# Optimization experiments

Hardware: AMD Instinct MI355X
Metric: run time of the kernel (lower is better)

The kernel has to match this reference:

```python
import math
import jax, jax.numpy as jnp
import numpy as np

N_HEAD = 8


def setup_inputs() -> dict:
    key = jax.random.key(0)
    ks = jax.random.split(key, 9)
    B, S, D = 4, 2048, 512
    s = 1.0 / math.sqrt(D)
    return {
        "x": jax.random.normal(ks[0], (B, S, D), jnp.float32),
        "Wq": jax.random.normal(ks[1], (D, D), jnp.float32) * s,
        "bq": jax.random.normal(ks[2], (D,), jnp.float32) * s,
        "Wk": jax.random.normal(ks[3], (D, D), jnp.float32) * s,
        "bk": jax.random.normal(ks[4], (D,), jnp.float32) * s,
        "Wv": jax.random.normal(ks[5], (D, D), jnp.float32) * s,
        "bv": jax.random.normal(ks[6], (D,), jnp.float32) * s,
        "Wo": jax.random.normal(ks[7], (D, D), jnp.float32) * s,
        "bo": jax.random.normal(ks[8], (D,), jnp.float32) * s,
    }


def reference(x, Wq, bq, Wk, bk, Wv, bv, Wo, bo):
    B, S, D = x.shape
    H = N_HEAD
    hd = D // H
    # projections -> [B, H, S, hd]
    def split_heads(y):
        return y.reshape(B, S, H, hd).transpose(0, 2, 1, 3)
    q = split_heads(x @ Wq + bq)
    k = split_heads(x @ Wk + bk)
    v = split_heads(x @ Wv + bv)
    scale = 1.0 / math.sqrt(hd)
    scores = jnp.einsum("bhqd,bhkd->bhqk", q, k) * scale  # [B,H,S,S]
    attn = jax.nn.softmax(scores, axis=-1)
    ctx = jnp.einsum("bhqk,bhkd->bhqd", attn, v)  # [B,H,S,hd]
    ctx = ctx.transpose(0, 2, 1, 3).reshape(B, S, D)
    out = ctx @ Wo + bo
    avg_attn = attn.mean(axis=1)  # [B,S,S]
    return out, avg_attn
```

## Files before the change

### kernel.cpp

```cpp
#include <hip/hip_runtime.h>

typedef __bf16 bf16;
typedef __bf16 bf16x8 __attribute__((ext_vector_type(8)));
typedef float  f32x4  __attribute__((ext_vector_type(4)));
typedef float  f32x16 __attribute__((ext_vector_type(16)));
typedef unsigned u32x4 __attribute__((ext_vector_type(4)));

#define MFMA16(a,b,c) __builtin_amdgcn_mfma_f32_16x16x32_bf16((a),(b),(c),0,0,0)
#define MFMA32(a,b,c) __builtin_amdgcn_mfma_f32_32x32x16_bf16((a),(b),(c),0,0,0)

#define BATCH 4
#define SEQ   2048
#define DIM   512
#define NH    8
#define HD    64
#define QSCALE 0.18033688f

__device__ __forceinline__ bf16x8 ldsfrag(const bf16* t, int row, int kc, int quad){
    int unit = ((kc << 2) + quad) ^ (row & 7);
    return *(const bf16x8*)(t + row * 64 + unit * 8);
}
__device__ __forceinline__ bf16x8 ldsfrag32(const bf16* t, int row, int unit){
    return *(const bf16x8*)(t + row * 64 + ((unit ^ (row & 7)) << 3));
}

__device__ __forceinline__ void stage64x64(const bf16* src, long rowStride, bf16* dst, int tid){
#pragma unroll
    for (int rnd = 0; rnd < 2; ++rnd){
        int sid = tid + rnd * 256;
        int row = sid >> 3, s = sid & 7;
        bf16x8 val = *(const bf16x8*)(src + (long)row * rowStride + s * 8);
        *(bf16x8*)(dst + row * 64 + ((s ^ (row & 7)) << 3)) = val;
    }
}

__device__ __forceinline__ unsigned packbf(float lo, float hi){
    unsigned short lb = __builtin_bit_cast(unsigned short, (bf16)lo);
    unsigned short hb = __builtin_bit_cast(unsigned short, (bf16)hi);
    return (unsigned)lb | ((unsigned)hb << 16);
}

__global__ __launch_bounds__(256) void cvt_x(const float* __restrict__ x, bf16* __restrict__ xb){
    int i = blockIdx.x * 256 + threadIdx.x;
    float4 f = ((const float4*)x)[i];
    bf16* o = xb + 4 * (long)i;
    o[0] = (bf16)f.x; o[1] = (bf16)f.y; o[2] = (bf16)f.z; o[3] = (bf16)f.w;
}

__global__ __launch_bounds__(256) void cvt_wt(const float* __restrict__ Wq, const float* __restrict__ Wk,
                                              const float* __restrict__ Wv, const float* __restrict__ Wo,
                                              bf16* __restrict__ WTb){
    int z = blockIdx.z;
    const float* W = (z == 0) ? Wq : (z == 1) ? Wk : (z == 2) ? Wv : Wo;
    bf16* WT = WTb + (long)z * DIM * DIM;
    __shared__ float lt[32 * 33];
    int t = threadIdx.x, r0 = t >> 5, c = t & 31;
    int k0 = blockIdx.x * 32, n0 = blockIdx.y * 32;
#pragma unroll
    for (int i = 0; i < 4; ++i){
        int row = r0 + i * 8;
        lt[row * 33 + c] = W[(long)(k0 + row) * DIM + n0 + c];
    }
    __syncthreads();
#pragma unroll
    for (int i = 0; i < 4; ++i){
        int nr = r0 + i * 8;
        WT[(long)(n0 + nr) * DIM + k0 + c] = (bf16)lt[c * 33 + nr];
    }
}

__global__ __launch_bounds__(256) void gemm_qkv(const bf16* __restrict__ X, const bf16* __restrict__ WTb,
                                                const float* __restrict__ bq, const float* __restrict__ bk,
                                                const float* __restrict__ bv, bf16* __restrict__ outb){
    __shared__ __align__(16) bf16 lA[128 * 64];
    __shared__ __align__(16) bf16 lB[128 * 64];
    int z = blockIdx.z;
    const bf16* WT = WTb + (long)z * DIM * DIM;
    const float* bias = (z == 0) ? bq : (z == 1) ? bk : bv;
    float qs = (z == 0) ? QSCALE : 1.0f;
    bf16* out = outb + (long)z * BATCH * SEQ * DIM;
    int tid = threadIdx.x, lane = tid & 63, w = tid >> 6;
    int wm = w >> 1, wn = w & 1;
    int m0 = blockIdx.y * 128, n0 = blockIdx.x * 128;
    int r16 = lane & 15, quad = lane >> 4;
    f32x4 zz = {0.f, 0.f, 0.f, 0.f};
    f32x4 acc[4][4];
#pragma unroll
    for (int a = 0; a < 4; ++a)
#pragma unroll
        for (int b2 = 0; b2 < 4; ++b2) acc[a][b2] = zz;

    for (int k0 = 0; k0 < DIM; k0 += 64){
        __syncthreads();
#pragma unroll
        for (int rnd = 0; rnd < 4; ++rnd){
            int sid = tid + rnd * 256;
            int row = sid >> 3, s = sid & 7;
            *(bf16x8*)(lA + row * 64 + ((s ^ (row & 7)) << 3)) =
                *(const bf16x8*)(X + (long)(m0 + row) * DIM + k0 + s * 8);
            *(bf16x8*)(lB + row * 64 + ((s ^ (row & 7)) << 3)) =
                *(const bf16x8*)(WT + (long)(n0 + row) * DIM + k0 + s * 8);
        }
        __syncthreads();
#pragma unroll
        for (int kc = 0; kc < 2; ++kc){
            bf16x8 aF[4], bF[4];
#pragma unroll
            for (int i = 0; i < 4; ++i){
                aF[i] = ldsfrag(lA, wm * 64 + i * 16 + r16, kc, quad);
                bF[i] = ldsfrag(lB, wn * 64 + i * 16 + r16, kc, quad);
            }
#pragma unroll
            for (int rb = 0; rb < 4; ++rb)
#pragma unroll
                for (int nb = 0; nb < 4; ++nb)
                    acc[rb][nb] = MFMA16(aF[rb], bF[nb], acc[rb][nb]);
        }
    }
#pragma unroll
    for (int nb = 0; nb < 4; ++nb){
        int col = n0 + wn * 64 + nb * 16 + r16;
        float bv_ = bias[col];
        int hh = col >> 6, d = col & 63;
#pragma unroll
        for (int rb = 0; rb < 4; ++rb)
#pragma unroll
            for (int r = 0; r < 4; ++r){
                int row = m0 + wm * 64 + rb * 16 + quad * 4 + r;
                int bb = row >> 11, s = row & 2047;
                out[((long)(bb * NH + hh) * SEQ + s) * HD + d] = (bf16)((acc[rb][nb][r] + bv_) * qs);
            }
    }
}

__global__ __launch_bounds__(256) void vtrans(const bf16* __restrict__ v, bf16* __restrict__ vT){
    __shared__ bf16 lt[64 * 72];
    int tid = threadIdx.x;
    int s0 = blockIdx.x * 64;
    int bh = blockIdx.z * NH + blockIdx.y;
#pragma unroll
    for (int rnd = 0; rnd < 2; ++rnd){
        int sid = tid + rnd * 256;
        int row = sid >> 3, sg = sid & 7;
        *(bf16x8*)(lt + row * 72 + sg * 8) =
            *(const bf16x8*)(v + ((long)bh * SEQ + s0 + row) * HD + sg * 8);
    }
    __syncthreads();
#pragma unroll
    for (int rnd = 0; rnd < 2; ++rnd){
        int sid = tid + rnd * 256;
        int d = sid >> 3, sg = sid & 7;
        bf16x8 o;
#pragma unroll
        for (int j = 0; j < 8; ++j) o[j] = lt[(sg * 8 + j) * 72 + d];
        *(bf16x8*)(vT + ((long)bh * HD + d) * SEQ + s0 + sg * 8) = o;
    }
}

__global__ __launch_bounds__(256) void attn_flash(const bf16* __restrict__ q, const bf16* __restrict__ k,
                                                  const bf16* __restrict__ vT, bf16* __restrict__ ctx,
                                                  float* __restrict__ llv_g){
    __shared__ __align__(16) bf16 lQ[128 * 64];
    __shared__ __align__(16) bf16 lK[64 * 64];
    __shared__ __align__(16) bf16 lV[64 * 64];
    int tid = threadIdx.x, lane = tid & 63, w = tid >> 6;
    int lin = blockIdx.x + (blockIdx.y << 4) + (blockIdx.z << 7);
    int task = ((lin & 7) << 6) + (lin >> 3);
    int qt = task & 15, h = (task >> 4) & 7, b = task >> 7;
    int bh = b * NH + h;
    int q0 = qt * 128;
    int row32 = lane & 31, half = lane >> 5;

    {
        const bf16* src = q + ((long)bh * SEQ + q0) * HD;
#pragma unroll
        for (int rnd = 0; rnd < 4; ++rnd){
            int sid = tid + rnd * 256;
            int row = sid >> 3, s = sid & 7;
            *(bf16x8*)(lQ + row * 64 + ((s ^ (row & 7)) << 3)) =
                *(const bf16x8*)(src + (long)row * HD + s * 8);
        }
    }
    __syncthreads();
    bf16x8 qF[4];
#pragma unroll
    for (int s = 0; s < 4; ++s) qF[s] = ldsfrag32(lQ, w * 32 + row32, 2 * s + half);

    f32x16 ctxacc[2];
#pragma unroll
    for (int i = 0; i < 16; ++i){ ctxacc[0][i] = 0.f; ctxacc[1][i] = 0.f; }
    float lsum = 0.f;

    int r0_ = tid >> 3, s_ = tid & 7;
    const bf16* kbase = k + (long)bh * SEQ * HD;
    const bf16* vbase = vT + (long)bh * HD * SEQ;
    bf16x8 kr0, kr1, vr0, vr1;

    auto LOADREGS = [&](int j0){
        kr0 = *(const bf16x8*)(kbase + (long)(j0 + r0_) * HD + s_ * 8);
        kr1 = *(const bf16x8*)(kbase + (long)(j0 + r0_ + 32) * HD + s_ * 8);
        vr0 = *(const bf16x8*)(vbase + (long)r0_ * SEQ + j0 + s_ * 8);
        vr1 = *(const bf16x8*)(vbase + (long)(r0_ + 32) * SEQ + j0 + s_ * 8);
    };
    auto WRITELDS = [&](){
        int u = (s_ ^ (r0_ & 7)) << 3;
        *(bf16x8*)(lK + r0_ * 64 + u) = kr0;
        *(bf16x8*)(lK + (r0_ + 32) * 64 + u) = kr1;
        *(bf16x8*)(lV + r0_ * 64 + u) = vr0;
        *(bf16x8*)(lV + (r0_ + 32) * 64 + u) = vr1;
    };
    auto COMPUTE = [&](){
        __builtin_amdgcn_s_setprio(1);
#pragma unroll
        for (int kb = 0; kb < 2; ++kb){
            f32x16 sacc;
#pragma unroll
            for (int i = 0; i < 16; ++i) sacc[i] = 0.f;
#pragma unroll
            for (int s = 0; s < 4; ++s)
                sacc = MFMA32(ldsfrag32(lK, kb * 32 + row32, 2 * s + half), qF[s], sacc);
            float p[16];
#pragma unroll
            for (int reg = 0; reg < 16; ++reg){
                p[reg] = __builtin_amdgcn_exp2f(sacc[reg]);
                lsum += p[reg];
            }
            unsigned Wp[4][2];
#pragma unroll
            for (int b2 = 0; b2 < 4; ++b2)
#pragma unroll
                for (int j = 0; j < 2; ++j)
                    Wp[b2][j] = packbf(p[4 * b2 + 2 * j], p[4 * b2 + 2 * j + 1]);
#pragma unroll
            for (int K = 0; K < 2; ++K){
                unsigned X0 = Wp[2 * K + 1][0], X1 = Wp[2 * K + 1][1];
                unsigned Y0 = Wp[2 * K][0],     Y1 = Wp[2 * K][1];
                unsigned X0p = (unsigned)__shfl_xor((int)X0, 32, 64);
                unsigned X1p = (unsigned)__shfl_xor((int)X1, 32, 64);
                unsigned Y0p = (unsigned)__shfl_xor((int)Y0, 32, 64);
                unsigned Y1p = (unsigned)__shfl_xor((int)Y1, 32, 64);
                u32x4 wv;
                wv[0] = half ? X0p : Y0;
                wv[1] = half ? X1p : Y1;
                wv[2] = half ? X0  : Y0p;
                wv[3] = half ? X1  : Y1p;
                bf16x8 pa = __builtin_bit_cast(bf16x8, wv);
                int ks = 2 * kb + K;
#pragma unroll
                for (int db = 0; db < 2; ++db)
                    ctxacc[db] = MFMA32(pa, ldsfrag32(lV, db * 32 + row32, 2 * ks + half), ctxacc[db]);
            }
        }
        __builtin_amdgcn_s_setprio(0);
    };

    LOADREGS(0);
    WRITELDS();
    __syncthreads();
    for (int j0 = 0; j0 < SEQ - 64; j0 += 64){
        LOADREGS(j0 + 64);
        COMPUTE();
        __syncthreads();
        WRITELDS();
        __syncthreads();
    }
    COMPUTE();

    lsum += __shfl_xor(lsum, 32, 64);
    float rv = 1.0f / lsum;
    float rinv[16];
#pragma unroll
    for (int reg = 0; reg < 16; ++reg){
        int qr = (reg & 3) + 8 * (reg >> 2) + 4 * half;
        rinv[reg] = __shfl(rv, qr, 64);
    }
#pragma unroll
    for (int db = 0; db < 2; ++db)
#pragma unroll
        for (int reg = 0; reg < 16; ++reg){
            int qr = (reg & 3) + 8 * (reg >> 2) + 4 * half;
            long srow = q0 + w * 32 + qr;
            ctx[((long)b * SEQ + srow) * DIM + h * HD + db * 32 + row32] =
                (bf16)(ctxacc[db][reg] * rinv[reg]);
        }
    if (half == 0)
        llv_g[(long)bh * SEQ + q0 + w * 32 + row32] = -__log2f(lsum) - 3.0f;
}

__global__ __launch_bounds__(256) void attn_avg(const bf16* __restrict__ q, const bf16* __restrict__ k,
                                                const float* __restrict__ llv_g, float* __restrict__ avg){
    __shared__ __align__(16) bf16 lQ[64 * 64];
    __shared__ __align__(16) bf16 lK[64 * 64];
    __shared__ __align__(16) float lsOut[4][16 * 65];
    int lin  = blockIdx.x + (blockIdx.y << 5) + (blockIdx.z << 10);
    int task = ((lin & 7) << 9) + (lin >> 3);
    int qt = task & 31;
    int jt = (task >> 5) & 31;
    int b  = task >> 10;
    int tid = threadIdx.x, lane = tid & 63, w = tid >> 6;
    int r16 = lane & 15, quad = lane >> 4;
    int qbase = qt * 64;
    int j0 = jt * 64;

    int r0_ = tid >> 3, s_ = tid & 7;
    int u_ = (s_ ^ (r0_ & 7)) << 3;
    bf16x8 qr0, qr1, kr0, kr1;
    auto LOADA = [&](int hh){
        long hA = (long)b * NH + hh;
        const bf16* qh = q + (hA * SEQ + qbase) * HD;
        const bf16* kh = k + (hA * SEQ + j0) * HD;
        qr0 = *(const bf16x8*)(qh + (long)r0_ * HD + s_ * 8);
        qr1 = *(const bf16x8*)(qh + (long)(r0_ + 32) * HD + s_ * 8);
        kr0 = *(const bf16x8*)(kh + (long)r0_ * HD + s_ * 8);
        kr1 = *(const bf16x8*)(kh + (long)(r0_ + 32) * HD + s_ * 8);
    };
    auto WRITEA = [&](){
        *(bf16x8*)(lQ + r0_ * 64 + u_) = qr0;
        *(bf16x8*)(lQ + (r0_ + 32) * 64 + u_) = qr1;
        *(bf16x8*)(lK + r0_ * 64 + u_) = kr0;
        *(bf16x8*)(lK + (r0_ + 32) * 64 + u_) = kr1;
    };

    f32x4 psum[4];
#pragma unroll
    for (int cb = 0; cb < 4; ++cb) psum[cb] = (f32x4){0.f, 0.f, 0.f, 0.f};

    LOADA(0);
    WRITEA();
    __syncthreads();
#pragma unroll 1
    for (int hh = 0; hh < NH; ++hh){
        if (hh < NH - 1) LOADA(hh + 1);
        f32x4 llv = *(const f32x4*)(llv_g + ((long)b * NH + hh) * SEQ + qbase + w * 16 + quad * 4);
        bf16x8 aF0 = ldsfrag(lQ, w * 16 + r16, 0, quad);
        bf16x8 aF1 = ldsfrag(lQ, w * 16 + r16, 1, quad);
#pragma unroll
        for (int cb = 0; cb < 4; ++cb){
            f32x4 sa = MFMA16(aF0, ldsfrag(lK, cb * 16 + r16, 0, quad), llv);
            sa = MFMA16(aF1, ldsfrag(lK, cb * 16 + r16, 1, quad), sa);
#pragma unroll
            for (int r = 0; r < 4; ++r)
                psum[cb][r] += __builtin_amdgcn_exp2f(sa[r]);
        }
        __syncthreads();
        if (hh < NH - 1){
            WRITEA();
            __syncthreads();
        }
    }

#pragma unroll
    for (int cb = 0; cb < 4; ++cb)
#pragma unroll
        for (int r = 0; r < 4; ++r)
            lsOut[w][(quad * 4 + r) * 65 + cb * 16 + r16] = psum[cb][r];
#pragma unroll
    for (int i = 0; i < 4; ++i){
        int row  = ((i >> 1) << 3) + (lane >> 3);
        int col4 = ((i & 1) << 5) + ((lane & 7) << 2);
        f32x4 v = *(const f32x4*)(&lsOut[w][row * 65 + col4]);
        __builtin_nontemporal_store(v,
            (f32x4*)&avg[((long)b * SEQ + qbase + w * 16 + row) * SEQ + j0 + col4]);
    }
}

__global__ __launch_bounds__(256) void gemm_out(const bf16* __restrict__ CTX, const bf16* __restrict__ WT,
                                                const float* __restrict__ bo, float* __restrict__ out){
    __shared__ __align__(16) bf16 lA[128 * 64];
    __shared__ __align__(16) bf16 lB[128 * 64];
    int tid = threadIdx.x, lane = tid & 63, w = tid >> 6;
    int wm = w >> 1, wn = w & 1;
    int m0 = blockIdx.y * 128, n0 = blockIdx.x * 128;
    int r16 = lane & 15, quad = lane >> 4;
    f32x4 zz = {0.f, 0.f, 0.f, 0.f};
    f32x4 acc[4][4];
#pragma unroll
    for (int a = 0; a < 4; ++a)
#pragma unroll
        for (int b2 = 0; b2 < 4; ++b2) acc[a][b2] = zz;

    for (int k0 = 0; k0 < DIM; k0 += 64){
        __syncthreads();
#pragma unroll
        for (int rnd = 0; rnd < 4; ++rnd){
            int sid = tid + rnd * 256;
            int row = sid >> 3, s = sid & 7;
            *(bf16x8*)(lA + row * 64 + ((s ^ (row & 7)) << 3)) =
                *(const bf16x8*)(CTX + (long)(m0 + row) * DIM + k0 + s * 8);
            *(bf16x8*)(lB + row * 64 + ((s ^ (row & 7)) << 3)) =
                *(const bf16x8*)(WT + (long)(n0 + row) * DIM + k0 + s * 8);
        }
        __syncthreads();
#pragma unroll
        for (int kc = 0; kc < 2; ++kc){
            bf16x8 aF[4], bF[4];
#pragma unroll
            for (int i = 0; i < 4; ++i){
                aF[i] = ldsfrag(lA, wm * 64 + i * 16 + r16, kc, quad);
                bF[i] = ldsfrag(lB, wn * 64 + i * 16 + r16, kc, quad);
            }
#pragma unroll
            for (int rb2 = 0; rb2 < 4; ++rb2)
#pragma unroll
                for (int nb = 0; nb < 4; ++nb)
                    acc[rb2][nb] = MFMA16(aF[rb2], bF[nb], acc[rb2][nb]);
        }
    }
#pragma unroll
    for (int nb = 0; nb < 4; ++nb){
        int col = n0 + wn * 64 + nb * 16 + r16;
        float bv_ = bo[col];
#pragma unroll
        for (int rb2 = 0; rb2 < 4; ++rb2)
#pragma unroll
            for (int r = 0; r < 4; ++r){
                int row = m0 + wm * 64 + rb2 * 16 + quad * 4 + r;
                out[(long)row * DIM + col] = acc[rb2][nb][r] + bv_;
            }
    }
}

extern "C" void kernel_launch(void* const* d_in, const int* in_sizes, int n_in,
                              void* d_out, int out_size, void* d_ws, size_t ws_size,
                              hipStream_t stream) {
    const float* x  = (const float*)d_in[0];
    const float* Wq = (const float*)d_in[1];
    const float* bq = (const float*)d_in[2];
    const float* Wk = (const float*)d_in[3];
    const float* bk = (const float*)d_in[4];
    const float* Wv = (const float*)d_in[5];
    const float* bv = (const float*)d_in[6];
    const float* Wo = (const float*)d_in[7];
    const float* bo = (const float*)d_in[8];
    float* out = (float*)d_out;

    char* ws = (char*)d_ws;
    bf16*  xb   = (bf16*)(ws);
    bf16*  WT   = (bf16*)(ws + 8388608);
    bf16*  qb   = (bf16*)(ws + 10485760);
    bf16*  kb   = qb + (long)BATCH * SEQ * DIM;
    bf16*  vb   = kb + (long)BATCH * SEQ * DIM;
    bf16*  vT   = (bf16*)(ws + 35651584);
    bf16*  ctx  = (bf16*)(ws + 44040192);
    float* llv  = (float*)(ws + 52428800);

    cvt_x    <<<4096, 256, 0, stream>>>(x, xb);
    cvt_wt   <<<dim3(16, 16, 4), 256, 0, stream>>>(Wq, Wk, Wv, Wo, WT);
    gemm_qkv <<<dim3(4, 64, 3), 256, 0, stream>>>(xb, WT, bq, bk, bv, qb);
    vtrans   <<<dim3(32, 8, 4), 256, 0, stream>>>(vb, vT);
    attn_flash<<<dim3(16, 8, 4), 256, 0, stream>>>(qb, kb, vT, ctx, llv);
    attn_avg <<<dim3(32, 32, 4), 256, 0, stream>>>(qb, kb, llv, out + (long)BATCH * SEQ * DIM);
    gemm_out <<<dim3(4, 64), 256, 0, stream>>>(ctx, WT + 3L * DIM * DIM, bo, out);
}
```

Before: 247.5 us.

## Split flash-attention key range across two wave groups with double-buffered LDS

Result: faster. 240.1 us (-3.0%).

```diff
diff --git a/kernel.cpp b/kernel.cpp
--- a/kernel.cpp
+++ b/kernel.cpp
@@ -157,13 +157,14 @@
     }
 }
 
-__global__ __launch_bounds__(256) void attn_flash(const bf16* __restrict__ q, const bf16* __restrict__ k,
+__global__ __launch_bounds__(512) void attn_flash(const bf16* __restrict__ q, const bf16* __restrict__ k,
                                                   const bf16* __restrict__ vT, bf16* __restrict__ ctx,
                                                   float* __restrict__ llv_g){
     __shared__ __align__(16) bf16 lQ[128 * 64];
-    __shared__ __align__(16) bf16 lK[64 * 64];
-    __shared__ __align__(16) bf16 lV[64 * 64];
+    __shared__ __align__(16) bf16 lKV[2][2][8192];
     int tid = threadIdx.x, lane = tid & 63, w = tid >> 6;
+    int g = w >> 2, wq = w & 3;
+    int t256 = tid & 255;
     int lin = blockIdx.x + (blockIdx.y << 4) + (blockIdx.z << 7);
     int task = ((lin & 7) << 6) + (lin >> 3);
     int qt = task & 15, h = (task >> 4) & 7, b = task >> 7;
@@ -171,45 +172,52 @@
     int q0 = qt * 128;
     int row32 = lane & 31, half = lane >> 5;
 
-    {
-        const bf16* src = q + ((long)bh * SEQ + q0) * HD;
-#pragma unroll
-        for (int rnd = 0; rnd < 4; ++rnd){
-            int sid = tid + rnd * 256;
-            int row = sid >> 3, s = sid & 7;
-            *(bf16x8*)(lQ + row * 64 + ((s ^ (row & 7)) << 3)) =
-                *(const bf16x8*)(src + (long)row * HD + s * 8);
-        }
-    }
-    __syncthreads();
-    bf16x8 qF[4];
-#pragma unroll
-    for (int s = 0; s < 4; ++s) qF[s] = ldsfrag32(lQ, w * 32 + row32, 2 * s + half);
-
-    f32x16 ctxacc[2];
-#pragma unroll
-    for (int i = 0; i < 16; ++i){ ctxacc[0][i] = 0.f; ctxacc[1][i] = 0.f; }
-    float lsum = 0.f;
-
-    int r0_ = tid >> 3, s_ = tid & 7;
-    const bf16* kbase = k + (long)bh * SEQ * HD;
-    const bf16* vbase = vT + (long)bh * HD * SEQ;
+    int r0_ = t256 >> 3, s_ = t256 & 7;
+    const bf16* kbase = k + ((long)bh * SEQ + g * (SEQ / 2)) * HD;
+    const bf16* vbase = vT + (long)bh * HD * SEQ + g * (SEQ / 2);
     bf16x8 kr0, kr1, vr0, vr1;
 
-    auto LOADREGS = [&](int j0){
+    auto LOADREGS = [&](int jt){
+        int j0 = jt * 64;
         kr0 = *(const bf16x8*)(kbase + (long)(j0 + r0_) * HD + s_ * 8);
         kr1 = *(const bf16x8*)(kbase + (long)(j0 + r0_ + 32) * HD + s_ * 8);
         vr0 = *(const bf16x8*)(vbase + (long)r0_ * SEQ + j0 + s_ * 8);
         vr1 = *(const bf16x8*)(vbase + (long)(r0_ + 32) * SEQ + j0 + s_ * 8);
     };
-    auto WRITELDS = [&](){
+    auto WRITELDS = [&](int buf){
+        bf16* lK = lKV[g][buf];
+        bf16* lV = lK + 4096;
         int u = (s_ ^ (r0_ & 7)) << 3;
         *(bf16x8*)(lK + r0_ * 64 + u) = kr0;
         *(bf16x8*)(lK + (r0_ + 32) * 64 + u) = kr1;
         *(bf16x8*)(lV + r0_ * 64 + u) = vr0;
         *(bf16x8*)(lV + (r0_ + 32) * 64 + u) = vr1;
     };
-    auto COMPUTE = [&](){
+
+    LOADREGS(0);
+    {
+        const bf16* src = q + ((long)bh * SEQ + q0) * HD;
+#pragma unroll
+        for (int rnd = 0; rnd < 2; ++rnd){
+            int sid = tid + rnd * 512;
+            int row = sid >> 3, s = sid & 7;
+            *(bf16x8*)(lQ + row * 64 + ((s ^ (row & 7)) << 3)) =
+                *(const bf16x8*)(src + (long)row * HD + s * 8);
+        }
+    }
+    __syncthreads();
+    bf16x8 qF[4];
+#pragma unroll
+    for (int s = 0; s < 4; ++s) qF[s] = ldsfrag32(lQ, wq * 32 + row32, 2 * s + half);
+
+    f32x16 ctxacc[2];
+#pragma unroll
+    for (int i = 0; i < 16; ++i){ ctxacc[0][i] = 0.f; ctxacc[1][i] = 0.f; }
+    float lsum = 0.f;
+
+    auto COMPUTE = [&](int buf){
+        const bf16* lK = lKV[g][buf];
+        const bf16* lV = lK + 4096;
         __builtin_amdgcn_s_setprio(1);
 #pragma unroll
         for (int kb = 0; kb < 2; ++kb){
@@ -254,37 +262,51 @@
         __builtin_amdgcn_s_setprio(0);
     };
 
-    LOADREGS(0);
-    WRITELDS();
-    __syncthreads();
-    for (int j0 = 0; j0 < SEQ - 64; j0 += 64){
-        LOADREGS(j0 + 64);
-        COMPUTE();
-        __syncthreads();
-        WRITELDS();
-        __syncthreads();
-    }
-    COMPUTE();
-
-    lsum += __shfl_xor(lsum, 32, 64);
-    float rv = 1.0f / lsum;
-    float rinv[16];
-#pragma unroll
-    for (int reg = 0; reg < 16; ++reg){
-        int qr = (reg & 3) + 8 * (reg >> 2) + 4 * half;
-        rinv[reg] = __shfl(rv, qr, 64);
-    }
-#pragma unroll
-    for (int db = 0; db < 2; ++db)
+    WRITELDS(0);
+    __syncthreads();
+#pragma unroll 1
+    for (int t = 0; t < 15; ++t){
+        LOADREGS(t + 1);
+        COMPUTE(t & 1);
+        WRITELDS((t + 1) & 1);
+        __syncthreads();
+    }
+    COMPUTE(1);
+
+    __syncthreads();
+    float* xch = (float*)&lKV[0][0][0];
+    if (g == 1){
+        float* dst = xch + ((wq << 6) + lane) * 33;
+#pragma unroll
+        for (int i = 0; i < 16; ++i){ dst[i] = ctxacc[0][i]; dst[16 + i] = ctxacc[1][i]; }
+        dst[32] = lsum;
+    }
+    __syncthreads();
+    if (g == 0){
+        const float* src2 = xch + ((wq << 6) + lane) * 33;
+#pragma unroll
+        for (int i = 0; i < 16; ++i){ ctxacc[0][i] += src2[i]; ctxacc[1][i] += src2[16 + i]; }
+        lsum += src2[32];
+        lsum += __shfl_xor(lsum, 32, 64);
+        float rv = 1.0f / lsum;
+        float rinv[16];
 #pragma unroll
         for (int reg = 0; reg < 16; ++reg){
             int qr = (reg & 3) + 8 * (reg >> 2) + 4 * half;
-            long srow = q0 + w * 32 + qr;
-            ctx[((long)b * SEQ + srow) * DIM + h * HD + db * 32 + row32] =
-                (bf16)(ctxacc[db][reg] * rinv[reg]);
-        }
-    if (half == 0)
-        llv_g[(long)bh * SEQ + q0 + w * 32 + row32] = -__log2f(lsum) - 3.0f;
+            rinv[reg] = __shfl(rv, qr, 64);
+        }
+#pragma unroll
+        for (int db = 0; db < 2; ++db)
+#pragma unroll
+            for (int reg = 0; reg < 16; ++reg){
+                int qr = (reg & 3) + 8 * (reg >> 2) + 4 * half;
+                long srow = q0 + wq * 32 + qr;
+                ctx[((long)b * SEQ + srow) * DIM + h * HD + db * 32 + row32] =
+                    (bf16)(ctxacc[db][reg] * rinv[reg]);
+            }
+        if (half == 0)
+            llv_g[(long)bh * SEQ + q0 + wq * 32 + row32] = -__log2f(lsum) - 3.0f;
+    }
 }
 
 __global__ __launch_bounds__(256) void attn_avg(const bf16* __restrict__ q, const bf16* __restrict__ k,
@@ -448,7 +470,7 @@
     cvt_wt   <<<dim3(16, 16, 4), 256, 0, stream>>>(Wq, Wk, Wv, Wo, WT);
     gemm_qkv <<<dim3(4, 64, 3), 256, 0, stream>>>(xb, WT, bq, bk, bv, qb);
     vtrans   <<<dim3(32, 8, 4), 256, 0, stream>>>(vb, vT);
-    attn_flash<<<dim3(16, 8, 4), 256, 0, stream>>>(qb, kb, vT, ctx, llv);
+    attn_flash<<<dim3(16, 8, 4), 512, 0, stream>>>(qb, kb, vT, ctx, llv);
     attn_avg <<<dim3(32, 32, 4), 256, 0, stream>>>(qb, kb, llv, out + (long)BATCH * SEQ * DIM);
     gemm_out <<<dim3(4, 64), 256, 0, stream>>>(ctx, WT + 3L * DIM * DIM, bo, out);
 }
```
